# Kernel optimization log

Measured on AMD Instinct MI355X. Metric: run time of the kernel, lower is better.

The kernel has to match this reference:

```python
import jax, jax.numpy as jnp
import numpy as np

# 3x3 Gaussian smoothing kernel (symmetric, so correlation == convolution)
GAUSS = jnp.array([[1., 2., 1.], [2., 4., 2.], [1., 2., 1.]], dtype=jnp.float32) / 16.0


def _per_sample_conv_valid(x, k):
    """Per-sample 3x3 cross-correlation. x: [B,H,W], k: [B,3,3] -> [B,H-2,W-2].

    Implemented as a grouped conv treating batch as channels (groups=B),
    matching F.conv2d(pred.permute(1,0,2,3), weight=k[:,None], groups=B).
    """
    B = x.shape[0]
    out = jax.lax.conv_general_dilated(
        x[None],            # [1, B, H, W]
        k[:, None],         # [B, 1, 3, 3]
        window_strides=(1, 1), padding='VALID',
        dimension_numbers=('NCHW', 'OIHW', 'NCHW'),
        feature_group_count=B)
    return out[0]


def _gauss_blur_same(x):
    """SAME-padded 3x3 Gaussian smoothing. x: [B,h,w] -> [B,h,w]."""
    out = jax.lax.conv_general_dilated(
        x[:, None],                 # [B,1,h,w]
        GAUSS[None, None],          # [1,1,3,3]
        window_strides=(1, 1), padding='SAME',
        dimension_numbers=('NCHW', 'OIHW', 'NCHW'))
    return out[:, 0]


def setup_inputs() -> dict:
    key = jax.random.key(0)
    k1, k2, k3, k4 = jax.random.split(key, 4)
    B, H, W = 256, 256, 256
    pred = jax.random.normal(k1, (B, H, W), dtype=jnp.float32)
    rhs = jax.random.normal(k2, (B, H - 2, W - 2), dtype=jnp.float32)
    Laplace_kernel = jax.random.normal(k3, (B, 3, 3), dtype=jnp.float32)
    Df_dr_kernel = jax.random.normal(k4, (B, 3, 3), dtype=jnp.float32)
    RR = jnp.arange(B * H * W, dtype=jnp.float32).reshape(B, H, W)
    ZZ = jnp.arange(B * H * W, dtype=jnp.float32).reshape(B, H, W)
    return {"pred": pred, "rhs": rhs, "Laplace_kernel": Laplace_kernel,
            "Df_dr_kernel": Df_dr_kernel, "RR": RR, "ZZ": ZZ}


def reference(pred, rhs, Laplace_kernel, Df_dr_kernel, RR, ZZ):
    # Finite-difference Grad-Shafranov operator (per-sample stencils).
    Lpsi = _per_sample_conv_valid(pred, Laplace_kernel)          # [B,H-2,W-2]
    Dpsi_dr = -_per_sample_conv_valid(pred, Df_dr_kernel)        # [B,H-2,W-2]
    RR_in = RR[:, 1:-1, 1:-1]
    Dpsi_dr = Dpsi_dr / RR_in
    GS_ope = Lpsi - Dpsi_dr

    # Grid spacings and normalization alfa / (hr^2 * hz^2)
    hr = RR[:, 1, 2] - RR[:, 1, 1]                               # [B]
    hz = ZZ[:, 2, 1] - ZZ[:, 1, 1]                               # [B]
    alfa = -2.0 * (hr ** 2 + hz ** 2)
    scale = (alfa / (hr ** 2 * hz ** 2))[:, None, None]
    GS_ope = GS_ope * scale

    # Gaussian smoothing then MSE against rhs
    GS_ope = _gauss_blur_same(GS_ope)
    return jnp.mean((GS_ope - rhs) ** 2)
```

## Files before the change

kernel.cpp:

```cpp
#include <hip/hip_runtime.h>

#define HW 256
#define OW 254
#define RSTRIP 6
#define NSTRIPS 43
#define NWAVES (256 * NSTRIPS)
#define NBLOCK (NWAVES / 4)
#define NGS (RSTRIP + 2)
#define NOUT (256.0f * 254.0f * 254.0f)

__device__ __forceinline__ void load_row8(const float* __restrict__ base, int row,
                                          int cL, int c0, int cB, float* p) {
    p[0] = base[row * HW + cL];
    float4 v0 = *(const float4*)&base[row * HW + c0];
    p[1] = v0.x; p[2] = v0.y; p[3] = v0.z; p[4] = v0.w;
    float4 v1 = *(const float4*)&base[row * HW + cB];
    p[5] = v1.x; p[6] = v1.y; p[7] = v1.z;
}

__device__ __forceinline__ void load_rr6(const float* __restrict__ RRb, int row,
                                         int c0, float* rq) {
    float4 q0 = *(const float4*)&RRb[row * HW + c0];
    rq[0] = q0.x; rq[1] = q0.y; rq[2] = q0.z; rq[3] = q0.w;
    float2 q1 = *(const float2*)&RRb[row * HW + c0 + 4];
    rq[4] = q1.x; rq[5] = q1.y;
}

__device__ __forceinline__ void load_rhs4v(const float* __restrict__ rhsb, int row,
                                           int c0, int c2, float* rh) {
    float2 a = *(const float2*)&rhsb[row * OW + c0];
    float2 b = *(const float2*)&rhsb[row * OW + c2];
    rh[0] = a.x; rh[1] = a.y; rh[2] = b.x; rh[3] = b.y;
}

__device__ __forceinline__ float uniformf(float x) {
    return __int_as_float(__builtin_amdgcn_readfirstlane(__float_as_int(x)));
}

__global__ __launch_bounds__(256, 1) void pde_loss_main(
    const float* __restrict__ pred, const float* __restrict__ rhs,
    const float* __restrict__ Lk,   const float* __restrict__ Dk,
    const float* __restrict__ RR,   const float* __restrict__ ZZ,
    float* __restrict__ partial)
{
    const int tid  = threadIdx.x;
    const int lane = tid & 63;
    const int wv   = tid >> 6;
    const int gw   = blockIdx.x * 4 + wv;
    const int b    = gw / NSTRIPS;
    const int strip= gw - b * NSTRIPS;
    const int r0   = strip * RSTRIP;
    const int r1   = min(r0 + RSTRIP, OW);

    const float* predb = pred + (size_t)b * (HW * HW);
    const float* RRb   = RR   + (size_t)b * (HW * HW);
    const float* ZZb   = ZZ   + (size_t)b * (HW * HW);
    const float* rhsb  = rhs  + (size_t)b * (OW * OW);

    float kl[9], kd[9];
    #pragma unroll
    for (int q = 0; q < 9; q++) {
        kl[q] = uniformf(Lk[b * 9 + q]);
        kd[q] = uniformf(Dk[b * 9 + q]);
    }
    float hr = RRb[1 * HW + 2] - RRb[1 * HW + 1];
    float hz = ZZb[2 * HW + 1] - ZZb[1 * HW + 1];
    float hr2 = hr * hr, hz2 = hz * hz;
    const float scale = uniformf((-2.0f * (hr2 + hz2)) / (hr2 * hz2));

    const int c0 = lane * 4;
    const int cL = max(c0 - 1, 0);
    const int cB = min(c0 + 4, HW - 4);
    const int c2 = min(c0 + 2, OW - 4);

    float p[NGS + 2][8];
    #pragma unroll
    for (int s = 0; s < NGS + 2; ++s)
        load_row8(predb, min(max(r0 - 1 + s, 0), HW - 1), cL, c0, cB, p[s]);
    float rq[NGS][6];
    #pragma unroll
    for (int s = 0; s < NGS; ++s)
        load_rr6(RRb, min(max(r0 + s, 1), HW - 2), c0, rq[s]);
    float rh[RSTRIP][4];
    #pragma unroll
    for (int s = 0; s < RSTRIP; ++s)
        load_rhs4v(rhsb, min(r0 + s, OW - 1), c0, c2, rh[s]);

    __builtin_amdgcn_sched_barrier(0);

    float P[4] = {0, 0, 0, 0};
    float Q[4] = {0, 0, 0, 0};
    float acc = 0.0f;

    #pragma unroll
    for (int s = 0; s < NGS; ++s) {
        const int g = r0 - 1 + s;
        const bool rowok = (g >= 0) && (g < OW);

        float gs[6];
        #pragma unroll
        for (int u = 0; u < 6; ++u) {
            float sL = 0.0f, sD = 0.0f;
            #pragma unroll
            for (int kx = 0; kx < 3; ++kx) {
                sL = fmaf(p[s][u + kx],     kl[kx],     sL);
                sL = fmaf(p[s + 1][u + kx], kl[3 + kx], sL);
                sL = fmaf(p[s + 2][u + kx], kl[6 + kx], sL);
                sD = fmaf(p[s][u + kx],     kd[kx],     sD);
                sD = fmaf(p[s + 1][u + kx], kd[3 + kx], sD);
                sD = fmaf(p[s + 2][u + kx], kd[6 + kx], sD);
            }
            float gval = scale * fmaf(sD, __builtin_amdgcn_rcpf(rq[s][u]), sL);
            int x = c0 - 1 + u;
            gs[u] = (rowok && x >= 0 && x < OW) ? gval : 0.0f;
        }

        float hb[4];
        #pragma unroll
        for (int t = 0; t < 4; ++t)
            hb[t] = gs[t] + 2.0f * gs[t + 1] + gs[t + 2];

        const int i = g - 1;
        const bool iok = (s >= 2) && (i < r1);
        const float* rhrow = rh[(s >= 2) ? (s - 2) : 0];
        #pragma unroll
        for (int t = 0; t < 4; ++t) {
            float F = (P[t] + hb[t]) * (1.0f / 16.0f);
            float d = F - rhrow[t];
            acc += (iok && (c0 + t) < OW) ? d * d : 0.0f;
        }

        #pragma unroll
        for (int t = 0; t < 4; ++t) {
            P[t] = Q[t] + 2.0f * hb[t];
            Q[t] = hb[t];
        }
    }

    #pragma unroll
    for (int off = 32; off > 0; off >>= 1)
        acc += __shfl_down(acc, off, 64);
    __shared__ float sw[4];
    if (lane == 0) sw[wv] = acc;
    __syncthreads();
    if (tid == 0)
        partial[blockIdx.x] = sw[0] + sw[1] + sw[2] + sw[3];
}

__global__ __launch_bounds__(256) void pde_loss_reduce(
    const float* __restrict__ partial, int n, float* __restrict__ out)
{
    float acc = 0.0f;
    for (int i = threadIdx.x; i < n; i += 256) acc += partial[i];
    #pragma unroll
    for (int off = 32; off > 0; off >>= 1)
        acc += __shfl_down(acc, off, 64);
    __shared__ float sw[4];
    if ((threadIdx.x & 63) == 0) sw[threadIdx.x >> 6] = acc;
    __syncthreads();
    if (threadIdx.x == 0)
        out[0] = (sw[0] + sw[1] + sw[2] + sw[3]) / NOUT;
}

extern "C" void kernel_launch(void* const* d_in, const int* in_sizes, int n_in,
                              void* d_out, int out_size, void* d_ws, size_t ws_size,
                              hipStream_t stream) {
    const float* pred = (const float*)d_in[0];
    const float* rhs  = (const float*)d_in[1];
    const float* Lk   = (const float*)d_in[2];
    const float* Dk   = (const float*)d_in[3];
    const float* RR   = (const float*)d_in[4];
    const float* ZZ   = (const float*)d_in[5];
    float* out = (float*)d_out;
    float* partial = (float*)d_ws;

    pde_loss_main<<<NBLOCK, 256, 0, stream>>>(pred, rhs, Lk, Dk, RR, ZZ, partial);
    pde_loss_reduce<<<1, 256, 0, stream>>>(partial, NBLOCK, out);
}
```

Measured before the change: 224.7 us.

## Stream rows through rolling register buffers with prefetch and higher occupancy

Instead of loading the whole strip of pred, RR and rhs rows up front, rows are now loaded one step ahead inside the loop. They go into small rotating register buffers, with sched barriers so the loads overlap the stencil math. The strip height grows from 6 to 8, making 32 strips per sample so the sample and strip indices come from shifts. Launch bounds go from 1 to 4 blocks per CU to allow more occupancy. Boundary selects are replaced by multiplicative masks, and the right-edge load is split to stay in bounds; this reduces register pressure but depends on the prefetch distance being enough to hide memory latency.

```diff
diff --git a/kernel.cpp b/kernel.cpp
--- a/kernel.cpp
+++ b/kernel.cpp
@@ -2,20 +2,26 @@
 
 #define HW 256
 #define OW 254
-#define RSTRIP 6
-#define NSTRIPS 43
+#define RSTRIP 8
+#define NSTRIPS 32
 #define NWAVES (256 * NSTRIPS)
 #define NBLOCK (NWAVES / 4)
 #define NGS (RSTRIP + 2)
 #define NOUT (256.0f * 254.0f * 254.0f)
 
-__device__ __forceinline__ void load_row8(const float* __restrict__ base, int row,
-                                          int cL, int c0, int cB, float* p) {
-    p[0] = base[row * HW + cL];
-    float4 v0 = *(const float4*)&base[row * HW + c0];
+__device__ __forceinline__ float uniformf(float x) {
+    return __int_as_float(__builtin_amdgcn_readfirstlane(__float_as_int(x)));
+}
+
+__device__ __forceinline__ void load_p8(const float* __restrict__ base, int row,
+                                        int cL, int c0, int cB2, int cB3, float* p) {
+    const float* r = base + row * HW;
+    p[0] = r[cL];
+    float4 v0 = *(const float4*)&r[c0];
     p[1] = v0.x; p[2] = v0.y; p[3] = v0.z; p[4] = v0.w;
-    float4 v1 = *(const float4*)&base[row * HW + cB];
-    p[5] = v1.x; p[6] = v1.y; p[7] = v1.z;
+    float2 v1 = *(const float2*)&r[cB2];
+    p[5] = v1.x; p[6] = v1.y;
+    p[7] = r[cB3];
 }
 
 __device__ __forceinline__ void load_rr6(const float* __restrict__ RRb, int row,
@@ -33,11 +39,7 @@
     rh[0] = a.x; rh[1] = a.y; rh[2] = b.x; rh[3] = b.y;
 }
 
-__device__ __forceinline__ float uniformf(float x) {
-    return __int_as_float(__builtin_amdgcn_readfirstlane(__float_as_int(x)));
-}
-
-__global__ __launch_bounds__(256, 1) void pde_loss_main(
+__global__ __launch_bounds__(256, 4) void pde_loss_main(
     const float* __restrict__ pred, const float* __restrict__ rhs,
     const float* __restrict__ Lk,   const float* __restrict__ Dk,
     const float* __restrict__ RR,   const float* __restrict__ ZZ,
@@ -46,9 +48,9 @@
     const int tid  = threadIdx.x;
     const int lane = tid & 63;
     const int wv   = tid >> 6;
-    const int gw   = blockIdx.x * 4 + wv;
-    const int b    = gw / NSTRIPS;
-    const int strip= gw - b * NSTRIPS;
+    const int gw   = __builtin_amdgcn_readfirstlane(blockIdx.x * 4 + wv);
+    const int b    = gw >> 5;
+    const int strip= gw & 31;
     const int r0   = strip * RSTRIP;
     const int r1   = min(r0 + RSTRIP, OW);
 
@@ -68,25 +70,29 @@
     float hr2 = hr * hr, hz2 = hz * hz;
     const float scale = uniformf((-2.0f * (hr2 + hz2)) / (hr2 * hz2));
 
-    const int c0 = lane * 4;
-    const int cL = max(c0 - 1, 0);
-    const int cB = min(c0 + 4, HW - 4);
-    const int c2 = min(c0 + 2, OW - 4);
-
-    float p[NGS + 2][8];
-    #pragma unroll
-    for (int s = 0; s < NGS + 2; ++s)
-        load_row8(predb, min(max(r0 - 1 + s, 0), HW - 1), cL, c0, cB, p[s]);
-    float rq[NGS][6];
-    #pragma unroll
-    for (int s = 0; s < NGS; ++s)
-        load_rr6(RRb, min(max(r0 + s, 1), HW - 2), c0, rq[s]);
-    float rh[RSTRIP][4];
-    #pragma unroll
-    for (int s = 0; s < RSTRIP; ++s)
-        load_rhs4v(rhsb, min(r0 + s, OW - 1), c0, c2, rh[s]);
-
-    __builtin_amdgcn_sched_barrier(0);
+    const int c0  = lane * 4;
+    const int cL  = max(c0 - 1, 0);
+    const int cB2 = min(c0 + 4, HW - 2);
+    const int cB3 = min(c0 + 6, HW - 1);
+    const int c2  = min(c0 + 2, OW - 4);
+
+    float cm[6];
+    #pragma unroll
+    for (int u = 0; u < 6; ++u) {
+        int x = c0 - 1 + u;
+        cm[u] = (x >= 0 && x < OW) ? 1.0f : 0.0f;
+    }
+    const float am2 = (c0 + 2 < OW) ? 1.0f : 0.0f;
+    const float am3 = (c0 + 3 < OW) ? 1.0f : 0.0f;
+
+    float p[5][8];
+    float rqv[2][6];
+    float rhv[2][4];
+
+    #pragma unroll
+    for (int s = 0; s < 4; ++s)
+        load_p8(predb, min(max(r0 - 1 + s, 0), HW - 1), cL, c0, cB2, cB3, p[s]);
+    load_rr6(RRb, min(max(r0, 1), HW - 2), c0, rqv[0]);
 
     float P[4] = {0, 0, 0, 0};
     float Q[4] = {0, 0, 0, 0};
@@ -94,47 +100,64 @@
 
     #pragma unroll
     for (int s = 0; s < NGS; ++s) {
+        if (s <= 7)
+            load_p8(predb, min(r0 + 3 + s, HW - 1), cL, c0, cB2, cB3, p[(s + 4) % 5]);
+        if (s <= 8)
+            load_rr6(RRb, min(r0 + s + 1, HW - 2), c0, rqv[(s + 1) & 1]);
+        if (s >= 1 && s <= 8)
+            load_rhs4v(rhsb, min(r0 + s - 1, OW - 1), c0, c2, rhv[(s + 1) & 1]);
+        __builtin_amdgcn_sched_barrier(0);
+
         const int g = r0 - 1 + s;
-        const bool rowok = (g >= 0) && (g < OW);
-
-        float gs[6];
-        #pragma unroll
-        for (int u = 0; u < 6; ++u) {
-            float sL = 0.0f, sD = 0.0f;
+        const float rowm = (g >= 0 && g < OW) ? 1.0f : 0.0f;
+
+        const float* pa  = p[s % 5];
+        const float* pb2 = p[(s + 1) % 5];
+        const float* pc2 = p[(s + 2) % 5];
+        const float* rqs = rqv[s & 1];
+
+        float hb[4];
+        {
+            float gs[6];
             #pragma unroll
-            for (int kx = 0; kx < 3; ++kx) {
-                sL = fmaf(p[s][u + kx],     kl[kx],     sL);
-                sL = fmaf(p[s + 1][u + kx], kl[3 + kx], sL);
-                sL = fmaf(p[s + 2][u + kx], kl[6 + kx], sL);
-                sD = fmaf(p[s][u + kx],     kd[kx],     sD);
-                sD = fmaf(p[s + 1][u + kx], kd[3 + kx], sD);
-                sD = fmaf(p[s + 2][u + kx], kd[6 + kx], sD);
+            for (int u = 0; u < 6; ++u) {
+                float sL = 0.0f, sD = 0.0f;
+                #pragma unroll
+                for (int kx = 0; kx < 3; ++kx) {
+                    sL = fmaf(pa[u + kx],  kl[kx],     sL);
+                    sL = fmaf(pb2[u + kx], kl[3 + kx], sL);
+                    sL = fmaf(pc2[u + kx], kl[6 + kx], sL);
+                    sD = fmaf(pa[u + kx],  kd[kx],     sD);
+                    sD = fmaf(pb2[u + kx], kd[3 + kx], sD);
+                    sD = fmaf(pc2[u + kx], kd[6 + kx], sD);
+                }
+                float gval = scale * fmaf(sD, __builtin_amdgcn_rcpf(rqs[u]), sL);
+                gs[u] = gval * (cm[u] * rowm);
             }
-            float gval = scale * fmaf(sD, __builtin_amdgcn_rcpf(rq[s][u]), sL);
-            int x = c0 - 1 + u;
-            gs[u] = (rowok && x >= 0 && x < OW) ? gval : 0.0f;
+            #pragma unroll
+            for (int t = 0; t < 4; ++t)
+                hb[t] = gs[t] + 2.0f * gs[t + 1] + gs[t + 2];
         }
 
-        float hb[4];
-        #pragma unroll
-        for (int t = 0; t < 4; ++t)
-            hb[t] = gs[t] + 2.0f * gs[t + 1] + gs[t + 2];
-
-        const int i = g - 1;
-        const bool iok = (s >= 2) && (i < r1);
-        const float* rhrow = rh[(s >= 2) ? (s - 2) : 0];
+        if (s >= 2) {
+            const float rowaccm = ((r0 + s - 2) < r1) ? 1.0f : 0.0f;
+            const float* rhrow = rhv[s & 1];
+            #pragma unroll
+            for (int t = 0; t < 4; ++t) {
+                float F = (P[t] + hb[t]) * (1.0f / 16.0f);
+                float d = (F - rhrow[t]) * rowaccm;
+                if (t == 2) d *= am2;
+                if (t == 3) d *= am3;
+                acc = fmaf(d, d, acc);
+            }
+        }
+
         #pragma unroll
         for (int t = 0; t < 4; ++t) {
-            float F = (P[t] + hb[t]) * (1.0f / 16.0f);
-            float d = F - rhrow[t];
-            acc += (iok && (c0 + t) < OW) ? d * d : 0.0f;
-        }
-
-        #pragma unroll
-        for (int t = 0; t < 4; ++t) {
-            P[t] = Q[t] + 2.0f * hb[t];
+            P[t] = fmaf(2.0f, hb[t], Q[t]);
             Q[t] = hb[t];
         }
+        __builtin_amdgcn_sched_barrier(0);
     }
 
     #pragma unroll
```

Measured after the change: 232.1 us. +3.3%, slower.
